# Kernel optimization log

Measured on AMD Instinct MI355X. Metric: run time of the kernel, lower is better.

## Reference

```python
import jax, jax.numpy as jnp
import numpy as np

N_NODES = 50000
IN_F = 512
OUT_F = 512
N_EDGES = 1600000
DROP_P = 0.5
NEG_SLOPE = 0.01  # torch LeakyReLU default


def leaky_relu(x):
    return jnp.where(x >= 0, x, NEG_SLOPE * x)


def setup_inputs() -> dict:
    key = jax.random.key(0)
    k1, k2, k3, k4, k5, k6 = jax.random.split(key, 6)
    x = jax.random.normal(k1, (N_NODES, IN_F), dtype=jnp.float32)
    W = jax.random.normal(k2, (OUT_F, IN_F), dtype=jnp.float32) * (1.0 / np.sqrt(IN_F))
    # inverted dropout mask: bernoulli(keep)/keep, keep = 1 - p
    keep = 1.0 - DROP_P
    drop_mask = (jax.random.uniform(k3, (N_NODES, IN_F)) < keep).astype(jnp.float32) / keep
    adj_vals = jax.random.uniform(k4, (N_EDGES,), dtype=jnp.float32)
    adj_rows = jax.random.randint(k5, (N_EDGES,), 0, N_NODES, dtype=jnp.int32)
    adj_cols = jax.random.randint(k6, (N_EDGES,), 0, N_NODES, dtype=jnp.int32)
    return {"x": x, "W": W, "drop_mask": drop_mask, "adj_vals": adj_vals,
            "adj_rows": adj_rows, "adj_cols": adj_cols}


def reference(x, W, drop_mask, adj_vals, adj_rows, adj_cols):
    # support = Linear(dropout(x)); Linear weight is [out, in] (torch convention)
    support = jnp.einsum('ni,oi->no', x * drop_mask, W)  # [N, out]
    h = leaky_relu(support)
    # sparse adj @ h: out[r] += v * h[c]
    msgs = adj_vals[:, None] * h[adj_cols]               # [E, out]
    agg = jax.ops.segment_sum(msgs, adj_rows, num_segments=N_NODES)
    return leaky_relu(agg)
```

## Files before the change

kernel.cpp:

```cpp
#include <hip/hip_runtime.h>

#define NROWS 50000
#define NFEAT 512
#define NEDGE 1600000
#define SLOPE 0.01f

typedef unsigned short u16;
typedef __attribute__((ext_vector_type(8))) short short8;
typedef __attribute__((ext_vector_type(4))) float f32x4;
typedef __attribute__((ext_vector_type(4))) int i32x4;
typedef __attribute__((ext_vector_type(8))) unsigned short u16x8;

__device__ __forceinline__ u16 f2bf(float f) {
  unsigned u = __float_as_uint(f);
  u += 0x7fffu + ((u >> 16) & 1u);
  return (u16)(u >> 16);
}
__device__ __forceinline__ float lrelu(float v) { return v >= 0.f ? v : SLOPE * v; }

__device__ __forceinline__ void gload_lds16(const u16* g, u16* l) {
  __builtin_amdgcn_global_load_lds((const __attribute__((address_space(1))) void*)g,
                                   (__attribute__((address_space(3))) void*)l, 16, 0, 0);
}

__global__ void prep_kernel(const float* __restrict__ x, const float* __restrict__ m,
                            u16* __restrict__ xd, const float* __restrict__ w,
                            u16* __restrict__ wb, const int* __restrict__ rows,
                            int* __restrict__ counts) {
  const int stride = gridDim.x * blockDim.x;
  const int tid0 = blockIdx.x * blockDim.x + threadIdx.x;
  for (int i = tid0; i < (NROWS * NFEAT) / 8; i += stride) {
    size_t b = (size_t)i * 2;
    f32x4 a0 = __builtin_nontemporal_load(&((const f32x4*)x)[b]);
    f32x4 a1 = __builtin_nontemporal_load(&((const f32x4*)x)[b + 1]);
    f32x4 m0 = __builtin_nontemporal_load(&((const f32x4*)m)[b]);
    f32x4 m1 = __builtin_nontemporal_load(&((const f32x4*)m)[b + 1]);
    u16x8 o;
    o[0] = f2bf(a0[0] * m0[0]); o[1] = f2bf(a0[1] * m0[1]);
    o[2] = f2bf(a0[2] * m0[2]); o[3] = f2bf(a0[3] * m0[3]);
    o[4] = f2bf(a1[0] * m1[0]); o[5] = f2bf(a1[1] * m1[1]);
    o[6] = f2bf(a1[2] * m1[2]); o[7] = f2bf(a1[3] * m1[3]);
    *(u16x8*)(xd + (size_t)i * 8) = o;
  }
  for (int i = tid0; i < (NFEAT * NFEAT) / 8; i += stride) {
    size_t b = (size_t)i * 2;
    f32x4 a0 = __builtin_nontemporal_load(&((const f32x4*)w)[b]);
    f32x4 a1 = __builtin_nontemporal_load(&((const f32x4*)w)[b + 1]);
    u16x8 o;
    o[0] = f2bf(a0[0]); o[1] = f2bf(a0[1]); o[2] = f2bf(a0[2]); o[3] = f2bf(a0[3]);
    o[4] = f2bf(a1[0]); o[5] = f2bf(a1[1]); o[6] = f2bf(a1[2]); o[7] = f2bf(a1[3]);
    *(u16x8*)(wb + (size_t)i * 8) = o;
  }
  for (int i = tid0; i < NEDGE / 4; i += stride) {
    i32x4 r4 = __builtin_nontemporal_load(&((const i32x4*)rows)[i]);
    atomicAdd(&counts[r4[0]], 1);
    atomicAdd(&counts[r4[1]], 1);
    atomicAdd(&counts[r4[2]], 1);
    atomicAdd(&counts[r4[3]], 1);
  }
}

__global__ void scan_kernel(const int* __restrict__ counts, int* __restrict__ offs) {
  __shared__ int wpre[17];
  const int t = threadIdx.x;
  const int lane = t & 63, w = t >> 6;
  const int beg = t * 64;
  i32x4 c4[16];
  int s = 0;
  if (beg < NROWS) {
#pragma unroll
    for (int g = 0; g < 16; ++g) {
      int idx = beg + g * 4;
      if (idx < NROWS) {
        c4[g] = ((const i32x4*)counts)[idx >> 2];
        s += c4[g][0] + c4[g][1] + c4[g][2] + c4[g][3];
      }
    }
  }
  int inc = s;
#pragma unroll
  for (int d = 1; d < 64; d <<= 1) {
    int u = __shfl_up(inc, d);
    if (lane >= d) inc += u;
  }
  if (lane == 63) wpre[w + 1] = inc;
  __syncthreads();
  if (t == 0) {
    wpre[0] = 0;
    for (int i = 1; i <= 16; ++i) wpre[i] += wpre[i - 1];
    offs[NROWS] = wpre[16];
  }
  __syncthreads();
  int run = wpre[w] + inc - s;
  if (beg < NROWS) {
#pragma unroll
    for (int g = 0; g < 16; ++g) {
      int idx = beg + g * 4;
      if (idx < NROWS) {
        i32x4 o;
        o[0] = run; run += c4[g][0];
        o[1] = run; run += c4[g][1];
        o[2] = run; run += c4[g][2];
        o[3] = run; run += c4[g][3];
        ((i32x4*)offs)[idx >> 2] = o;
      }
    }
  }
}

__global__ void scatter_kernel(const float* __restrict__ vals, const int* __restrict__ rows,
                               const int* __restrict__ cols, const int* __restrict__ offs,
                               int* __restrict__ cursor, unsigned* __restrict__ svc) {
  int e0 = (blockIdx.x * blockDim.x + threadIdx.x) * 4;
  if (e0 >= NEDGE) return;
  i32x4 r4 = __builtin_nontemporal_load((const i32x4*)(rows + e0));
  i32x4 c4 = __builtin_nontemporal_load((const i32x4*)(cols + e0));
  f32x4 v4 = __builtin_nontemporal_load((const f32x4*)(vals + e0));
#pragma unroll
  for (int j = 0; j < 4; ++j) {
    int p = offs[r4[j]] + atomicAdd(&cursor[r4[j]], 1);
    svc[p] = ((unsigned)c4[j] << 16) | (unsigned)f2bf(v4[j]);
  }
}

__global__ __launch_bounds__(256) void gemm_kernel(const u16* __restrict__ xd,
                                                   const u16* __restrict__ wb,
                                                   unsigned char* __restrict__ hq,
                                                   float* __restrict__ scaleg) {
  __shared__ __align__(16) u16 lA[128 * 64];
  __shared__ float wmax[2][128];
  __shared__ float rinv[128];
  const int tid = threadIdx.x;
  const int lane = tid & 63;
  const int wid = tid >> 6;
  const int wm = wid >> 1, wn = wid & 1;
  const int bx0 = blockIdx.x;
  const int xcd = bx0 & 7, idx = bx0 >> 3;
  const int wg = (xcd < 4 ? xcd * 196 : 784 + (xcd - 4) * 195) + idx;
  const int tm = wg >> 2;
  const int tn = wg & 3;
  const long rowBase = (long)tm * 128;

  f32x4 acc[4][4] = {};

  const int sl8 = lane >> 3;
  const int scol = ((lane & 7) ^ sl8) * 8;
  const int rsel = lane & 15, kgrp = (lane >> 4) * 8;
  const u16* bbase = wb + ((long)(tn * 128 + wn * 64 + rsel)) * 512 + kgrp;

  for (int k0 = 0; k0 < 512; k0 += 64) {
    __syncthreads();
#pragma unroll
    for (int c = 0; c < 4; ++c) {
      int rbase = wid * 32 + c * 8;
      long gr = rowBase + rbase + sl8;
      if (gr > NROWS - 1) gr = NROWS - 1;
      gload_lds16(xd + gr * 512 + k0 + scol, lA + rbase * 64);
    }
    short8 b[4][2];
#pragma unroll
    for (int n = 0; n < 4; ++n) {
#pragma unroll
      for (int kk = 0; kk < 2; ++kk)
        b[n][kk] = *(const short8*)(bbase + (long)n * 16 * 512 + k0 + kk * 32);
    }
    __syncthreads();
    short8 a[4][2];
#pragma unroll
    for (int m = 0; m < 4; ++m) {
      int ar = wm * 64 + m * 16 + rsel;
      const u16* base = lA + ar * 64;
      int sw = (ar & 7) << 3;
      a[m][0] = *(const short8*)(base + (kgrp ^ sw));
      a[m][1] = *(const short8*)(base + ((32 + kgrp) ^ sw));
    }
#pragma unroll
    for (int kk = 0; kk < 2; ++kk)
#pragma unroll
      for (int m = 0; m < 4; ++m)
#pragma unroll
        for (int n = 0; n < 4; ++n)
          acc[m][n] = __builtin_amdgcn_mfma_f32_16x16x32_bf16(a[m][kk], b[n][kk], acc[m][n], 0, 0, 0);
  }

  const int crow = (lane >> 4) * 4;
  const int ccol = lane & 15;

  float pm[4][4];
#pragma unroll
  for (int m = 0; m < 4; ++m)
#pragma unroll
    for (int r2 = 0; r2 < 4; ++r2) {
      float mx = 0.f;
#pragma unroll
      for (int n = 0; n < 4; ++n) mx = fmaxf(mx, fabsf(lrelu(acc[m][n][r2])));
      pm[m][r2] = mx;
    }
#pragma unroll
  for (int d = 1; d < 16; d <<= 1)
#pragma unroll
    for (int m = 0; m < 4; ++m)
#pragma unroll
      for (int r2 = 0; r2 < 4; ++r2) pm[m][r2] = fmaxf(pm[m][r2], __shfl_xor(pm[m][r2], d));
  if ((lane & 15) == 0) {
#pragma unroll
    for (int m = 0; m < 4; ++m)
#pragma unroll
      for (int r2 = 0; r2 < 4; ++r2) wmax[wn][wm * 64 + m * 16 + crow + r2] = pm[m][r2];
  }
  __syncthreads();
  if (tid < 128) {
    float rm = fmaxf(wmax[0][tid], wmax[1][tid]);
    float s = rm > 0.f ? rm * (1.f / 127.f) : 1.f;
    rinv[tid] = rm > 0.f ? 127.f / rm : 0.f;
    long gr = rowBase + tid;
    if (gr < NROWS) scaleg[gr * 4 + tn] = s;
  }
  __syncthreads();

  unsigned char* lT = (unsigned char*)lA;
#pragma unroll
  for (int m = 0; m < 4; ++m) {
    int row0 = wm * 64 + m * 16 + crow;
    float ri0 = rinv[row0], ri1 = rinv[row0 + 1], ri2 = rinv[row0 + 2], ri3 = rinv[row0 + 3];
#pragma unroll
    for (int n = 0; n < 4; ++n) {
      int col = wn * 64 + n * 16 + ccol;
      float q0 = rintf(lrelu(acc[m][n][0]) * ri0);
      float q1 = rintf(lrelu(acc[m][n][1]) * ri1);
      float q2 = rintf(lrelu(acc[m][n][2]) * ri2);
      float q3 = rintf(lrelu(acc[m][n][3]) * ri3);
      int i0 = min(127, max(-127, (int)q0));
      int i1 = min(127, max(-127, (int)q1));
      int i2 = min(127, max(-127, (int)q2));
      int i3 = min(127, max(-127, (int)q3));
      unsigned pk = (i0 & 0xff) | ((i1 & 0xff) << 8) | ((i2 & 0xff) << 16) | ((i3 & 0xff) << 24);
#pragma unroll
      for (int r2 = 0; r2 < 4; ++r2) {
        int row = row0 + r2;
        lT[row * 128 + (col ^ ((row & 7) << 4))] = (unsigned char)(pk >> (8 * r2));
      }
    }
  }
  __syncthreads();
  {
    const int row = tid >> 1, seg = tid & 1;
    long gr = rowBase + row;
    if (gr < NROWS) {
      unsigned char* dst = hq + gr * 512 + tn * 128;
#pragma unroll
      for (int j = 0; j < 4; ++j) {
        int s = seg * 4 + j;
        i32x4 vv = *(const i32x4*)(lT + row * 128 + ((s ^ (row & 7)) << 4));
        *(i32x4*)(dst + s * 16) = vv;
      }
    }
  }
}

__global__ __launch_bounds__(256) void aggregate_kernel(const unsigned char* __restrict__ hq,
                                                        const float* __restrict__ scaleg,
                                                        const unsigned* __restrict__ svc,
                                                        const int* __restrict__ offs,
                                                        float* __restrict__ out) {
  const int lane = threadIdx.x & 63;
  const int wid = threadIdx.x >> 6;
  const int r = blockIdx.x * 4 + wid;
  if (r >= NROWS) return;
  const int beg = offs[r], end = offs[r + 1];
  const int half = lane >> 5, sub = lane & 31;
  const int grp = sub >> 3;
  float a[16] = {};
  const unsigned char* hp = hq + sub * 16;
  unsigned cb[4], nb[4];
  const int n = end - beg;
  const int ng = n >> 3;
  if (ng > 0) {
#pragma unroll
    for (int k = 0; k < 4; ++k) cb[k] = svc[beg + 2 * k + half];
  }
  for (int g = 0; g < ng; ++g) {
    if (g + 1 < ng) {
#pragma unroll
      for (int k = 0; k < 4; ++k) nb[k] = svc[beg + (g + 1) * 8 + 2 * k + half];
    }
#pragma unroll
    for (int k = 0; k < 4; ++k) {
      float v = __uint_as_float(cb[k] << 16);
      size_t c = (size_t)(cb[k] >> 16);
      float vs = v * scaleg[c * 4 + grp];
      i32x4 q = *(const i32x4*)(hp + c * 512);
#pragma unroll
      for (int j = 0; j < 4; ++j) {
        unsigned qq = (unsigned)q[j];
        a[4 * j + 0] += vs * (float)(signed char)(qq);
        a[4 * j + 1] += vs * (float)(signed char)(qq >> 8);
        a[4 * j + 2] += vs * (float)(signed char)(qq >> 16);
        a[4 * j + 3] += vs * (float)(signed char)(qq >> 24);
      }
    }
    if (g + 1 < ng) {
#pragma unroll
      for (int k = 0; k < 4; ++k) cb[k] = nb[k];
    }
  }
  int e = beg + ng * 8;
  for (; e + 1 < end; e += 2) {
    unsigned u = svc[e + half];
    float v = __uint_as_float(u << 16);
    size_t c = (size_t)(u >> 16);
    float vs = v * scaleg[c * 4 + grp];
    i32x4 q = *(const i32x4*)(hp + c * 512);
#pragma unroll
    for (int j = 0; j < 4; ++j) {
      unsigned qq = (unsigned)q[j];
      a[4 * j + 0] += vs * (float)(signed char)(qq);
      a[4 * j + 1] += vs * (float)(signed char)(qq >> 8);
      a[4 * j + 2] += vs * (float)(signed char)(qq >> 16);
      a[4 * j + 3] += vs * (float)(signed char)(qq >> 24);
    }
  }
  if (e < end) {
    unsigned u = svc[e];
    float v = __uint_as_float(u << 16);
    size_t c = (size_t)(u >> 16);
    float vs = half ? 0.f : v * scaleg[c * 4 + grp];
    i32x4 q = *(const i32x4*)(hp + c * 512);
#pragma unroll
    for (int j = 0; j < 4; ++j) {
      unsigned qq = (unsigned)q[j];
      a[4 * j + 0] += vs * (float)(signed char)(qq);
      a[4 * j + 1] += vs * (float)(signed char)(qq >> 8);
      a[4 * j + 2] += vs * (float)(signed char)(qq >> 16);
      a[4 * j + 3] += vs * (float)(signed char)(qq >> 24);
    }
  }
#pragma unroll
  for (int j = 0; j < 16; ++j) a[j] += __shfl_xor(a[j], 32);
  if (half == 0) {
    float* op = out + (size_t)r * NFEAT + sub * 16;
#pragma unroll
    for (int j = 0; j < 4; ++j) {
      f32x4 o;
      o[0] = lrelu(a[4 * j + 0]);
      o[1] = lrelu(a[4 * j + 1]);
      o[2] = lrelu(a[4 * j + 2]);
      o[3] = lrelu(a[4 * j + 3]);
      *(f32x4*)(op + 4 * j) = o;
    }
  }
}

extern "C" void kernel_launch(void* const* d_in, const int* in_sizes, int n_in,
                              void* d_out, int out_size, void* d_ws, size_t ws_size,
                              hipStream_t stream) {
  const float* x = (const float*)d_in[0];
  const float* W = (const float*)d_in[1];
  const float* mask = (const float*)d_in[2];
  const float* vals = (const float*)d_in[3];
  const int* rows = (const int*)d_in[4];
  const int* cols = (const int*)d_in[5];
  float* out = (float*)d_out;
  char* ws = (char*)d_ws;

  const size_t o_xd = 0;
  const size_t o_hq = o_xd + 51200000;
  const size_t o_wb = o_hq + 25600000;
  const size_t o_scale = o_wb + 524288;
  const size_t o_counts = o_scale + 800000;
  const size_t o_cursor = o_counts + 200000;
  const size_t o_offs = o_cursor + 200000;
  const size_t o_svc = o_offs + 200064;

  u16* xd = (u16*)(ws + o_xd);
  unsigned char* hq = (unsigned char*)(ws + o_hq);
  u16* wb = (u16*)(ws + o_wb);
  float* scaleg = (float*)(ws + o_scale);
  int* counts = (int*)(ws + o_counts);
  int* cursor = (int*)(ws + o_cursor);
  int* offs = (int*)(ws + o_offs);
  unsigned* svc = (unsigned*)(ws + o_svc);

  hipMemsetAsync(counts, 0, 400000, stream);

  prep_kernel<<<2048, 256, 0, stream>>>(x, mask, xd, W, wb, rows, counts);
  scan_kernel<<<1, 1024, 0, stream>>>(counts, offs);
  scatter_kernel<<<1563, 256, 0, stream>>>(vals, rows, cols, offs, cursor, svc);
  gemm_kernel<<<391 * 4, 256, 0, stream>>>(xd, wb, hq, scaleg);
  aggregate_kernel<<<12500, 256, 0, stream>>>(hq, scaleg, svc, offs, out);
}
```

Measured before the change: 403.6 us.

## Fuse dropout and bf16 conversion of x into GEMM A-tile loading

Removes the separate pass that wrote a bf16 dropout-applied copy of x to workspace. The GEMM now reads fp32 x and the mask directly, multiplies and converts to bf16 in registers, and stores the result into a swizzled LDS tile. The block tiling also changes from 128 rows by 128 columns with 4 waves to 64 rows by all 512 columns with 8 waves, so each x row is read once instead of four times. This saves the intermediate write and re-read, but gives up the async global-to-LDS loads and adds an extra barrier per k-step. Each tile load now also carries twice the bytes, since it reads fp32 x plus the fp32 mask.

```diff
diff --git a/kernel.cpp b/kernel.cpp
--- a/kernel.cpp
+++ b/kernel.cpp
@@ -9,6 +9,7 @@
 typedef __attribute__((ext_vector_type(8))) short short8;
 typedef __attribute__((ext_vector_type(4))) float f32x4;
 typedef __attribute__((ext_vector_type(4))) int i32x4;
+typedef __attribute__((ext_vector_type(2))) unsigned uintx2;
 typedef __attribute__((ext_vector_type(8))) unsigned short u16x8;
 
 __device__ __forceinline__ u16 f2bf(float f) {
@@ -18,30 +19,10 @@
 }
 __device__ __forceinline__ float lrelu(float v) { return v >= 0.f ? v : SLOPE * v; }
 
-__device__ __forceinline__ void gload_lds16(const u16* g, u16* l) {
-  __builtin_amdgcn_global_load_lds((const __attribute__((address_space(1))) void*)g,
-                                   (__attribute__((address_space(3))) void*)l, 16, 0, 0);
-}
-
-__global__ void prep_kernel(const float* __restrict__ x, const float* __restrict__ m,
-                            u16* __restrict__ xd, const float* __restrict__ w,
-                            u16* __restrict__ wb, const int* __restrict__ rows,
-                            int* __restrict__ counts) {
+__global__ void prep_kernel(const float* __restrict__ w, u16* __restrict__ wb,
+                            const int* __restrict__ rows, int* __restrict__ counts) {
   const int stride = gridDim.x * blockDim.x;
   const int tid0 = blockIdx.x * blockDim.x + threadIdx.x;
-  for (int i = tid0; i < (NROWS * NFEAT) / 8; i += stride) {
-    size_t b = (size_t)i * 2;
-    f32x4 a0 = __builtin_nontemporal_load(&((const f32x4*)x)[b]);
-    f32x4 a1 = __builtin_nontemporal_load(&((const f32x4*)x)[b + 1]);
-    f32x4 m0 = __builtin_nontemporal_load(&((const f32x4*)m)[b]);
-    f32x4 m1 = __builtin_nontemporal_load(&((const f32x4*)m)[b + 1]);
-    u16x8 o;
-    o[0] = f2bf(a0[0] * m0[0]); o[1] = f2bf(a0[1] * m0[1]);
-    o[2] = f2bf(a0[2] * m0[2]); o[3] = f2bf(a0[3] * m0[3]);
-    o[4] = f2bf(a1[0] * m1[0]); o[5] = f2bf(a1[1] * m1[1]);
-    o[6] = f2bf(a1[2] * m1[2]); o[7] = f2bf(a1[3] * m1[3]);
-    *(u16x8*)(xd + (size_t)i * 8) = o;
-  }
   for (int i = tid0; i < (NFEAT * NFEAT) / 8; i += stride) {
     size_t b = (size_t)i * 2;
     f32x4 a0 = __builtin_nontemporal_load(&((const f32x4*)w)[b]);
@@ -123,40 +104,39 @@
   }
 }
 
-__global__ __launch_bounds__(256) void gemm_kernel(const u16* __restrict__ xd,
+__global__ __launch_bounds__(512) void gemm_kernel(const float* __restrict__ x,
+                                                   const float* __restrict__ msk,
                                                    const u16* __restrict__ wb,
                                                    unsigned char* __restrict__ hq,
                                                    float* __restrict__ scaleg) {
-  __shared__ __align__(16) u16 lA[128 * 64];
-  __shared__ float wmax[2][128];
-  __shared__ float rinv[128];
+  __shared__ __align__(16) char smem[64 * 512];
+  __shared__ float wmax[8][64];
+  __shared__ float rinv4[4][64];
+  u16* lA = (u16*)smem;
   const int tid = threadIdx.x;
   const int lane = tid & 63;
-  const int wid = tid >> 6;
-  const int wm = wid >> 1, wn = wid & 1;
-  const int bx0 = blockIdx.x;
-  const int xcd = bx0 & 7, idx = bx0 >> 3;
-  const int wg = (xcd < 4 ? xcd * 196 : 784 + (xcd - 4) * 195) + idx;
-  const int tm = wg >> 2;
-  const int tn = wg & 3;
-  const long rowBase = (long)tm * 128;
+  const int wv = tid >> 6;
+  const long rowBase = (long)blockIdx.x * 64;
 
   f32x4 acc[4][4] = {};
 
-  const int sl8 = lane >> 3;
-  const int scol = ((lane & 7) ^ sl8) * 8;
+  const int srow = tid >> 3;
+  const int sk8 = tid & 7;
+  const int swslot = (sk8 ^ (srow & 7)) * 8;
+  long sgr = rowBase + srow;
+  if (sgr > NROWS - 1) sgr = NROWS - 1;
+  const float* xp = x + sgr * 512 + sk8 * 8;
+  const float* mp = msk + sgr * 512 + sk8 * 8;
+  u16* swr = lA + srow * 64 + swslot;
+
   const int rsel = lane & 15, kgrp = (lane >> 4) * 8;
-  const u16* bbase = wb + ((long)(tn * 128 + wn * 64 + rsel)) * 512 + kgrp;
+  const u16* bbase = wb + ((long)(wv * 64 + rsel)) * 512 + kgrp;
 
   for (int k0 = 0; k0 < 512; k0 += 64) {
-    __syncthreads();
-#pragma unroll
-    for (int c = 0; c < 4; ++c) {
-      int rbase = wid * 32 + c * 8;
-      long gr = rowBase + rbase + sl8;
-      if (gr > NROWS - 1) gr = NROWS - 1;
-      gload_lds16(xd + gr * 512 + k0 + scol, lA + rbase * 64);
-    }
+    f32x4 xa = __builtin_nontemporal_load((const f32x4*)(xp + k0));
+    f32x4 xb = __builtin_nontemporal_load((const f32x4*)(xp + k0 + 4));
+    f32x4 ma = __builtin_nontemporal_load((const f32x4*)(mp + k0));
+    f32x4 mb = __builtin_nontemporal_load((const f32x4*)(mp + k0 + 4));
     short8 b[4][2];
 #pragma unroll
     for (int n = 0; n < 4; ++n) {
@@ -165,10 +145,17 @@
         b[n][kk] = *(const short8*)(bbase + (long)n * 16 * 512 + k0 + kk * 32);
     }
     __syncthreads();
+    u16x8 o;
+    o[0] = f2bf(xa[0] * ma[0]); o[1] = f2bf(xa[1] * ma[1]);
+    o[2] = f2bf(xa[2] * ma[2]); o[3] = f2bf(xa[3] * ma[3]);
+    o[4] = f2bf(xb[0] * mb[0]); o[5] = f2bf(xb[1] * mb[1]);
+    o[6] = f2bf(xb[2] * mb[2]); o[7] = f2bf(xb[3] * mb[3]);
+    *(u16x8*)swr = o;
+    __syncthreads();
     short8 a[4][2];
 #pragma unroll
     for (int m = 0; m < 4; ++m) {
-      int ar = wm * 64 + m * 16 + rsel;
+      int ar = m * 16 + rsel;
       const u16* base = lA + ar * 64;
       int sw = (ar & 7) << 3;
       a[m][0] = *(const short8*)(base + (kgrp ^ sw));
@@ -206,26 +193,30 @@
 #pragma unroll
     for (int m = 0; m < 4; ++m)
 #pragma unroll
-      for (int r2 = 0; r2 < 4; ++r2) wmax[wn][wm * 64 + m * 16 + crow + r2] = pm[m][r2];
-  }
-  __syncthreads();
-  if (tid < 128) {
-    float rm = fmaxf(wmax[0][tid], wmax[1][tid]);
+      for (int r2 = 0; r2 < 4; ++r2) wmax[wv][m * 16 + crow + r2] = pm[m][r2];
+  }
+  __syncthreads();
+  if (tid < 256) {
+    int g = tid >> 6, row = tid & 63;
+    float rm = fmaxf(wmax[2 * g][row], wmax[2 * g + 1][row]);
     float s = rm > 0.f ? rm * (1.f / 127.f) : 1.f;
-    rinv[tid] = rm > 0.f ? 127.f / rm : 0.f;
-    long gr = rowBase + tid;
-    if (gr < NROWS) scaleg[gr * 4 + tn] = s;
-  }
-  __syncthreads();
-
-  unsigned char* lT = (unsigned char*)lA;
+    rinv4[g][row] = rm > 0.f ? 127.f / rm : 0.f;
+    long gr = rowBase + row;
+    if (gr < NROWS) scaleg[gr * 4 + g] = s;
+  }
+  __syncthreads();
+
+  unsigned char* lT = (unsigned char*)smem;
+  const int qg = wv >> 1;
 #pragma unroll
   for (int m = 0; m < 4; ++m) {
-    int row0 = wm * 64 + m * 16 + crow;
-    float ri0 = rinv[row0], ri1 = rinv[row0 + 1], ri2 = rinv[row0 + 2], ri3 = rinv[row0 + 3];
+    int row0 = m * 16 + crow;
+    float ri0 = rinv4[qg][row0], ri1 = rinv4[qg][row0 + 1];
+    float ri2 = rinv4[qg][row0 + 2], ri3 = rinv4[qg][row0 + 3];
 #pragma unroll
     for (int n = 0; n < 4; ++n) {
-      int col = wn * 64 + n * 16 + ccol;
+      int col = wv * 64 + n * 16 + ccol;
+      int cg = col & 127;
       float q0 = rintf(lrelu(acc[m][n][0]) * ri0);
       float q1 = rintf(lrelu(acc[m][n][1]) * ri1);
       float q2 = rintf(lrelu(acc[m][n][2]) * ri2);
@@ -238,21 +229,22 @@
 #pragma unroll
       for (int r2 = 0; r2 < 4; ++r2) {
         int row = row0 + r2;
-        lT[row * 128 + (col ^ ((row & 7) << 4))] = (unsigned char)(pk >> (8 * r2));
+        lT[row * 512 + (qg << 7) + (cg ^ ((row & 7) << 4))] = (unsigned char)(pk >> (8 * r2));
       }
     }
   }
   __syncthreads();
   {
-    const int row = tid >> 1, seg = tid & 1;
+    const int row = tid >> 3, seg = tid & 7;
     long gr = rowBase + row;
     if (gr < NROWS) {
-      unsigned char* dst = hq + gr * 512 + tn * 128;
+      unsigned char* dst = hq + gr * 512;
 #pragma unroll
       for (int j = 0; j < 4; ++j) {
-        int s = seg * 4 + j;
-        i32x4 vv = *(const i32x4*)(lT + row * 128 + ((s ^ (row & 7)) << 4));
-        *(i32x4*)(dst + s * 16) = vv;
+        int gc = seg * 4 + j;
+        int g2 = gc >> 3, s = gc & 7;
+        i32x4 vv = *(const i32x4*)(lT + row * 512 + g2 * 128 + ((s ^ (row & 7)) << 4));
+        *(i32x4*)(dst + gc * 16) = vv;
       }
     }
   }
@@ -363,8 +355,7 @@
   float* out = (float*)d_out;
   char* ws = (char*)d_ws;
 
-  const size_t o_xd = 0;
-  const size_t o_hq = o_xd + 51200000;
+  const size_t o_hq = 0;
   const size_t o_wb = o_hq + 25600000;
   const size_t o_scale = o_wb + 524288;
   const size_t o_counts = o_scale + 800000;
@@ -372,7 +363,6 @@
   const size_t o_offs = o_cursor + 200000;
   const size_t o_svc = o_offs + 200064;
 
-  u16* xd = (u16*)(ws + o_xd);
   unsigned char* hq = (unsigned char*)(ws + o_hq);
   u16* wb = (u16*)(ws + o_wb);
   float* scaleg = (float*)(ws + o_scale);
@@ -383,9 +373,9 @@
 
   hipMemsetAsync(counts, 0, 400000, stream);
 
-  prep_kernel<<<2048, 256, 0, stream>>>(x, mask, xd, W, wb, rows, counts);
+  prep_kernel<<<1024, 256, 0, stream>>>(W, wb, rows, counts);
   scan_kernel<<<1, 1024, 0, stream>>>(counts, offs);
   scatter_kernel<<<1563, 256, 0, stream>>>(vals, rows, cols, offs, cursor, svc);
-  gemm_kernel<<<391 * 4, 256, 0, stream>>>(xd, wb, hq, scaleg);
+  gemm_kernel<<<782, 512, 0, stream>>>(x, mask, wb, hq, scaleg);
   aggregate_kernel<<<12500, 256, 0, stream>>>(hq, scaleg, svc, offs, out);
 }
```

Result: slower. 421.4 us (+4.4%).
